# Optimization experiments

Hardware: AMD Instinct MI355X
Metric: run time of the kernel (lower is better)

The kernel has to match this reference:

```python
import jax, jax.numpy as jnp
import numpy as np

S, D_MODEL, D_K = 4096, 1024, 64
SCALE = float(np.sqrt(D_K))


def setup_inputs() -> dict:
    key = jax.random.key(0)
    ks = jax.random.split(key, 7)
    def p(k, shape, fan_in):
        # torch nn.Linear default init: U(-1/sqrt(fan_in), 1/sqrt(fan_in))
        lim = 1.0 / np.sqrt(fan_in)
        return jax.random.uniform(k, shape, jnp.float32, -lim, lim)
    return {
        "x": jax.random.normal(ks[0], (S, D_MODEL), jnp.float32),
        "Wq": p(ks[1], (D_K, D_MODEL), D_MODEL),
        "bq": p(ks[2], (D_K,), D_MODEL),
        "Wk": p(ks[3], (D_K, D_MODEL), D_MODEL),
        "bk": p(ks[4], (D_K,), D_MODEL),
        "Wv": p(ks[5], (D_K, D_MODEL), D_MODEL),
        "bv": p(ks[6], (D_K,), D_MODEL),
    }


def reference(x, Wq, bq, Wk, bk, Wv, bv):
    # Linear projections: y = x @ W.T + b  (torch nn.Linear convention)
    Q = x @ Wq.T + bq          # [S, d_k]
    K = x @ Wk.T + bk          # [S, d_k]
    V = x @ Wv.T + bv          # [S, d_k]
    scores = (Q @ K.T) / SCALE  # [S, S]
    # causal mask: -inf strictly above the diagonal (triu(1))
    row = jnp.arange(S)[:, None]
    col = jnp.arange(S)[None, :]
    scores = jnp.where(col > row, -jnp.inf, scores)
    attn = jax.nn.softmax(scores, axis=1)
    return attn @ V            # [S, d_k]
```

## Files before the change

kernel.cpp:

```cpp
#include <hip/hip_runtime.h>

#define SS 4096
#define DM 1024

typedef __attribute__((ext_vector_type(4))) float f32x4;
typedef __attribute__((ext_vector_type(8))) __bf16 bf16x8;
typedef __attribute__((ext_vector_type(8))) unsigned short ushort8;
typedef __attribute__((ext_vector_type(4))) unsigned short ushort4v;

#define NEGHUGE -3.0e38f
#define LOG2E 1.44269504f

__device__ __forceinline__ unsigned short f2b(float f) {
    unsigned u = __builtin_bit_cast(unsigned, f);
    u += 0x7fffu + ((u >> 16) & 1u);
    return (unsigned short)(u >> 16);
}

__device__ __forceinline__ f32x4 mfma16(ushort8 a, ushort8 b, f32x4 c) {
    return __builtin_amdgcn_mfma_f32_16x16x32_bf16(
        __builtin_bit_cast(bf16x8, a), __builtin_bit_cast(bf16x8, b), c, 0, 0, 0);
}

__global__ __launch_bounds__(256) void convw_kernel(
    const float* __restrict__ Wq, const float* __restrict__ Wk,
    const float* __restrict__ Wv, unsigned short* __restrict__ wb)
{
    int i = (blockIdx.x * 256 + threadIdx.x) * 4;
    const float* src;
    if (i < 65536) src = Wq + i;
    else if (i < 131072) src = Wk + (i - 65536);
    else src = Wv + (i - 131072);
    f32x4 v = *reinterpret_cast<const f32x4*>(src);
    ushort4v o;
    o[0] = f2b(v[0]); o[1] = f2b(v[1]); o[2] = f2b(v[2]); o[3] = f2b(v[3]);
    *reinterpret_cast<ushort4v*>(wb + i) = o;
}

__global__ __launch_bounds__(512) void proj_kernel(
    const float* __restrict__ x, const unsigned short* __restrict__ wb,
    const float* __restrict__ bq, const float* __restrict__ bk, const float* __restrict__ bv,
    unsigned short* __restrict__ Qs, unsigned short* __restrict__ Kb,
    unsigned short* __restrict__ VT)
{
    __shared__ float comb[8 * 3072];
    const int m0 = blockIdx.x * 16;
    const int tid = threadIdx.x;
    const int w = tid >> 6, l = tid & 63;
    const int lc = l & 15;
    const int lk = (l >> 4) * 8;

    f32x4 acc[12] = {};
    const float* xrow = x + (m0 + lc) * DM;
    const int kbase = w * 128;

    for (int kk = 0; kk < 128; kk += 32) {
        const int k0 = kbase + kk + lk;
        f32x4 u = *reinterpret_cast<const f32x4*>(xrow + k0);
        f32x4 v = *reinterpret_cast<const f32x4*>(xrow + k0 + 4);
        ushort8 a;
        a[0] = f2b(u[0]); a[1] = f2b(u[1]); a[2] = f2b(u[2]); a[3] = f2b(u[3]);
        a[4] = f2b(v[0]); a[5] = f2b(v[1]); a[6] = f2b(v[2]); a[7] = f2b(v[3]);
#pragma unroll
        for (int nf = 0; nf < 12; nf++) {
            ushort8 b = *reinterpret_cast<const ushort8*>(wb + (nf * 16 + lc) * DM + k0);
            acc[nf] = mfma16(a, b, acc[nf]);
        }
    }

#pragma unroll
    for (int nf = 0; nf < 12; nf++)
#pragma unroll
        for (int r = 0; r < 4; r++) {
            int row = (l >> 4) * 4 + r;
            comb[w * 3072 + row * 192 + nf * 16 + lc] = acc[nf][r];
        }
    __syncthreads();

    for (int idx = tid; idx < 3072; idx += 512) {
        int row = idx / 192, col = idx % 192;
        float s = 0.f;
#pragma unroll
        for (int ww = 0; ww < 8; ww++) s += comb[ww * 3072 + idx];
        int grow = m0 + row;
        if (col < 64) {
            s += bq[col];
            Qs[grow * 64 + col] = f2b(s * 0.125f);
        } else if (col < 128) {
            s += bk[col - 64];
            Kb[grow * 64 + col - 64] = f2b(s);
        } else {
            s += bv[col - 128];
            VT[(col - 128) * SS + grow] = f2b(s);
        }
    }
}

__global__ __launch_bounds__(256) void attn_part_kernel(
    const unsigned short* __restrict__ Qs, const unsigned short* __restrict__ Kb,
    const unsigned short* __restrict__ VT, float* __restrict__ part)
{
    __shared__ unsigned short plds[4][16 * 64];
    __shared__ float comb[4][16 * 66];

    const int bid = blockIdx.x;
    const int g = bid >> 2, c = bid & 3;
    const int q0 = g * 16;
    const int tid = threadIdx.x;
    const int w = tid >> 6, l = tid & 63;
    const int lc = l & 15;
    const int lg4 = l >> 4;
    const int lk = lg4 * 8;

    const int T = g / 4 + 1;
    const int W0 = c * 4 + w;

    ushort8 aq0 = *reinterpret_cast<const ushort8*>(Qs + (q0 + lc) * 64 + lk);
    ushort8 aq1 = *reinterpret_cast<const ushort8*>(Qs + (q0 + lc) * 64 + 32 + lk);

    float m4[4], l4[4];
    f32x4 o[4] = {};
#pragma unroll
    for (int r = 0; r < 4; r++) { m4[r] = NEGHUGE; l4[r] = 0.f; }

    char* myp = reinterpret_cast<char*>(plds[w]);

    for (int t = W0; t < T; t += 16) {
        const int kv0 = t * 64;
        f32x4 s[4] = {};
#pragma unroll
        for (int nf = 0; nf < 4; nf++) {
            const unsigned short* kr = Kb + (kv0 + nf * 16 + lc) * 64;
            ushort8 b0 = *reinterpret_cast<const ushort8*>(kr + lk);
            ushort8 b1 = *reinterpret_cast<const ushort8*>(kr + 32 + lk);
            s[nf] = mfma16(aq0, b0, s[nf]);
            s[nf] = mfma16(aq1, b1, s[nf]);
        }
        if (kv0 + 63 > q0) {
#pragma unroll
            for (int nf = 0; nf < 4; nf++)
#pragma unroll
                for (int r = 0; r < 4; r++) {
                    int colg = kv0 + nf * 16 + lc;
                    int rowg = q0 + lg4 * 4 + r;
                    if (colg > rowg) s[nf][r] = NEGHUGE;
                }
        }
#pragma unroll
        for (int r = 0; r < 4; r++) {
            float mx = fmaxf(fmaxf(s[0][r], s[1][r]), fmaxf(s[2][r], s[3][r]));
            mx = fmaxf(mx, __shfl_xor(mx, 1));
            mx = fmaxf(mx, __shfl_xor(mx, 2));
            mx = fmaxf(mx, __shfl_xor(mx, 4));
            mx = fmaxf(mx, __shfl_xor(mx, 8));
            float mn = fmaxf(m4[r], mx);
            float sc = exp2f((m4[r] - mn) * LOG2E);
            m4[r] = mn;
            float rs = 0.f;
#pragma unroll
            for (int nf = 0; nf < 4; nf++) {
                float p = exp2f((s[nf][r] - mn) * LOG2E);
                s[nf][r] = p;
                rs += p;
            }
            rs += __shfl_xor(rs, 1);
            rs += __shfl_xor(rs, 2);
            rs += __shfl_xor(rs, 4);
            rs += __shfl_xor(rs, 8);
            l4[r] = l4[r] * sc + rs;
            o[0][r] *= sc; o[1][r] *= sc; o[2][r] *= sc; o[3][r] *= sc;
        }
#pragma unroll
        for (int nf = 0; nf < 4; nf++)
#pragma unroll
            for (int r = 0; r < 4; r++) {
                int row = lg4 * 4 + r;
                int byte = (row * 128 + (nf * 16 + lc) * 2) ^ ((row & 7) << 4);
                *reinterpret_cast<unsigned short*>(myp + byte) = f2b(s[nf][r]);
            }
        asm volatile("s_waitcnt lgkmcnt(0)" ::: "memory");
        __builtin_amdgcn_sched_barrier(0);
#pragma unroll
        for (int k = 0; k < 2; k++) {
            int rbyte = (lc * 128 + (k * 32 + lk) * 2) ^ ((lc & 7) << 4);
            ushort8 pa = *reinterpret_cast<const ushort8*>(myp + rbyte);
#pragma unroll
            for (int df = 0; df < 4; df++) {
                ushort8 bv = *reinterpret_cast<const ushort8*>(
                    VT + (df * 16 + lc) * SS + kv0 + k * 32 + lk);
                o[df] = mfma16(pa, bv, o[df]);
            }
        }
    }

#pragma unroll
    for (int df = 0; df < 4; df++)
#pragma unroll
        for (int r = 0; r < 4; r++)
            comb[w][(lg4 * 4 + r) * 66 + df * 16 + lc] = o[df][r];
    if (lc == 0) {
#pragma unroll
        for (int r = 0; r < 4; r++) {
            comb[w][(lg4 * 4 + r) * 66 + 64] = m4[r];
            comb[w][(lg4 * 4 + r) * 66 + 65] = l4[r];
        }
    }
    __syncthreads();

    float* pp = part + bid * 1056;
    for (int idx = tid; idx < 1024; idx += 256) {
        int row = idx >> 6, col = idx & 63;
        float M = fmaxf(fmaxf(comb[0][row * 66 + 64], comb[1][row * 66 + 64]),
                        fmaxf(comb[2][row * 66 + 64], comb[3][row * 66 + 64]));
        float val = 0.f, den = 0.f;
#pragma unroll
        for (int ww = 0; ww < 4; ww++) {
            float f = exp2f((comb[ww][row * 66 + 64] - M) * LOG2E);
            val += comb[ww][row * 66 + col] * f;
            den += comb[ww][row * 66 + 65] * f;
        }
        pp[row * 66 + col] = val;
        if (col == 0) {
            pp[row * 66 + 64] = M;
            pp[row * 66 + 65] = den;
        }
    }
}

__global__ __launch_bounds__(256) void attn_comb_kernel(
    const float* __restrict__ part, float* __restrict__ out)
{
    const int g = blockIdx.x;
    const int q0 = g * 16;
    const float* p0 = part + (g * 4) * 1056;
    for (int idx = threadIdx.x; idx < 1024; idx += 256) {
        int row = idx >> 6, col = idx & 63;
        float M = NEGHUGE;
#pragma unroll
        for (int cc = 0; cc < 4; cc++)
            M = fmaxf(M, p0[cc * 1056 + row * 66 + 64]);
        float val = 0.f, den = 0.f;
#pragma unroll
        for (int cc = 0; cc < 4; cc++) {
            float f = exp2f((p0[cc * 1056 + row * 66 + 64] - M) * LOG2E);
            val += p0[cc * 1056 + row * 66 + col] * f;
            den += p0[cc * 1056 + row * 66 + 65] * f;
        }
        out[(q0 + row) * 64 + col] = val / den;
    }
}

extern "C" void kernel_launch(void* const* d_in, const int* in_sizes, int n_in,
                              void* d_out, int out_size, void* d_ws, size_t ws_size,
                              hipStream_t stream) {
    const float* x  = (const float*)d_in[0];
    const float* Wq = (const float*)d_in[1];
    const float* bq = (const float*)d_in[2];
    const float* Wk = (const float*)d_in[3];
    const float* bk = (const float*)d_in[4];
    const float* Wv = (const float*)d_in[5];
    const float* bv = (const float*)d_in[6];
    float* out = (float*)d_out;

    char* ws = (char*)d_ws;
    unsigned short* wb = (unsigned short*)ws;
    unsigned short* Qs = (unsigned short*)(ws + 393216);
    unsigned short* Kb = (unsigned short*)(ws + 917504);
    unsigned short* VT = (unsigned short*)(ws + 1441792);
    float* part = (float*)(ws + 1966080);

    convw_kernel<<<dim3(192), dim3(256), 0, stream>>>(Wq, Wk, Wv, wb);
    proj_kernel<<<dim3(256), dim3(512), 0, stream>>>(x, wb, bq, bk, bv, Qs, Kb, VT);
    attn_part_kernel<<<dim3(1024), dim3(256), 0, stream>>>(Qs, Kb, VT, part);
    attn_comb_kernel<<<dim3(256), dim3(256), 0, stream>>>(part, out);
}
```

Baseline: 56.03 us.

## Split projection over feature groups, transpose attention MFMA layout, reverse block order

The projection kernel now runs 1024 smaller blocks of 256 threads, each computing 48 output features over a 16-row tile, instead of 256 blocks computing all 192. This cuts the shared-memory reduction size and raises occupancy, at the cost of reading x four times. The attention kernel computes S transposed so that each lane holds one query row, which removes most of the cross-lane shuffles. It prefetches V fragments before the softmax, packs P with padded LDS stores, and launches the heaviest causal query groups first to improve load balance.

```diff
diff --git a/kernel.cpp b/kernel.cpp
--- a/kernel.cpp
+++ b/kernel.cpp
@@ -2,11 +2,13 @@
 
 #define SS 4096
 #define DM 1024
+#define PSTRIDE 1056
 
 typedef __attribute__((ext_vector_type(4))) float f32x4;
 typedef __attribute__((ext_vector_type(8))) __bf16 bf16x8;
 typedef __attribute__((ext_vector_type(8))) unsigned short ushort8;
 typedef __attribute__((ext_vector_type(4))) unsigned short ushort4v;
+typedef __attribute__((ext_vector_type(2))) unsigned int uint2v;
 
 #define NEGHUGE -3.0e38f
 #define LOG2E 1.44269504f
@@ -37,24 +39,28 @@
     *reinterpret_cast<ushort4v*>(wb + i) = o;
 }
 
-__global__ __launch_bounds__(512) void proj_kernel(
+__global__ __launch_bounds__(256) void proj_kernel(
     const float* __restrict__ x, const unsigned short* __restrict__ wb,
     const float* __restrict__ bq, const float* __restrict__ bk, const float* __restrict__ bv,
     unsigned short* __restrict__ Qs, unsigned short* __restrict__ Kb,
     unsigned short* __restrict__ VT)
 {
-    __shared__ float comb[8 * 3072];
-    const int m0 = blockIdx.x * 16;
+    __shared__ float comb[4 * 16 * 52];
+    const int bid = blockIdx.x;
+    const int m0 = (bid >> 2) * 16;
+    const int fg = bid & 3;
     const int tid = threadIdx.x;
     const int w = tid >> 6, l = tid & 63;
     const int lc = l & 15;
-    const int lk = (l >> 4) * 8;
-
-    f32x4 acc[12] = {};
+    const int lg4 = l >> 4;
+    const int lk = lg4 * 8;
+
+    f32x4 acc[3] = {};
     const float* xrow = x + (m0 + lc) * DM;
-    const int kbase = w * 128;
-
-    for (int kk = 0; kk < 128; kk += 32) {
+    const unsigned short* wbase = wb + (fg * 48 + lc) * DM;
+    const int kbase = w * 256;
+
+    for (int kk = 0; kk < 256; kk += 32) {
         const int k0 = kbase + kk + lk;
         f32x4 u = *reinterpret_cast<const f32x4*>(xrow + k0);
         f32x4 v = *reinterpret_cast<const f32x4*>(xrow + k0 + 4);
@@ -62,36 +68,34 @@
         a[0] = f2b(u[0]); a[1] = f2b(u[1]); a[2] = f2b(u[2]); a[3] = f2b(u[3]);
         a[4] = f2b(v[0]); a[5] = f2b(v[1]); a[6] = f2b(v[2]); a[7] = f2b(v[3]);
 #pragma unroll
-        for (int nf = 0; nf < 12; nf++) {
-            ushort8 b = *reinterpret_cast<const ushort8*>(wb + (nf * 16 + lc) * DM + k0);
+        for (int nf = 0; nf < 3; nf++) {
+            ushort8 b = *reinterpret_cast<const ushort8*>(wbase + nf * 16 * DM + k0);
             acc[nf] = mfma16(a, b, acc[nf]);
         }
     }
 
 #pragma unroll
-    for (int nf = 0; nf < 12; nf++)
-#pragma unroll
-        for (int r = 0; r < 4; r++) {
-            int row = (l >> 4) * 4 + r;
-            comb[w * 3072 + row * 192 + nf * 16 + lc] = acc[nf][r];
-        }
+    for (int nf = 0; nf < 3; nf++)
+#pragma unroll
+        for (int r = 0; r < 4; r++)
+            comb[w * 832 + (lg4 * 4 + r) * 52 + nf * 16 + lc] = acc[nf][r];
     __syncthreads();
 
-    for (int idx = tid; idx < 3072; idx += 512) {
-        int row = idx / 192, col = idx % 192;
-        float s = 0.f;
-#pragma unroll
-        for (int ww = 0; ww < 8; ww++) s += comb[ww * 3072 + idx];
+    for (int idx = tid; idx < 768; idx += 256) {
+        int row = idx / 48, col = idx % 48;
+        int off = row * 52 + col;
+        float s = comb[off] + comb[832 + off] + comb[1664 + off] + comb[2496 + off];
         int grow = m0 + row;
-        if (col < 64) {
-            s += bq[col];
-            Qs[grow * 64 + col] = f2b(s * 0.125f);
-        } else if (col < 128) {
-            s += bk[col - 64];
-            Kb[grow * 64 + col - 64] = f2b(s);
+        int gcol = fg * 48 + col;
+        if (gcol < 64) {
+            s += bq[gcol];
+            Qs[grow * 64 + gcol] = f2b(s * 0.125f);
+        } else if (gcol < 128) {
+            s += bk[gcol - 64];
+            Kb[grow * 64 + gcol - 64] = f2b(s);
         } else {
-            s += bv[col - 128];
-            VT[(col - 128) * SS + grow] = f2b(s);
+            s += bv[gcol - 128];
+            VT[(gcol - 128) * SS + grow] = f2b(s);
         }
     }
 }
@@ -100,11 +104,12 @@
     const unsigned short* __restrict__ Qs, const unsigned short* __restrict__ Kb,
     const unsigned short* __restrict__ VT, float* __restrict__ part)
 {
-    __shared__ unsigned short plds[4][16 * 64];
-    __shared__ float comb[4][16 * 66];
+    __shared__ __align__(16) char plds[4 * 2304];
+    __shared__ float scomb[4][16 * 66];
 
     const int bid = blockIdx.x;
-    const int g = bid >> 2, c = bid & 3;
+    const int g = 255 - (bid >> 2);
+    const int c = bid & 3;
     const int q0 = g * 16;
     const int tid = threadIdx.x;
     const int w = tid >> 6, l = tid & 63;
@@ -118,12 +123,10 @@
     ushort8 aq0 = *reinterpret_cast<const ushort8*>(Qs + (q0 + lc) * 64 + lk);
     ushort8 aq1 = *reinterpret_cast<const ushort8*>(Qs + (q0 + lc) * 64 + 32 + lk);
 
-    float m4[4], l4[4];
+    float m4 = NEGHUGE, l4 = 0.f;
     f32x4 o[4] = {};
-#pragma unroll
-    for (int r = 0; r < 4; r++) { m4[r] = NEGHUGE; l4[r] = 0.f; }
-
-    char* myp = reinterpret_cast<char*>(plds[w]);
+
+    char* myp = plds + w * 2304;
 
     for (int t = W0; t < T; t += 16) {
         const int kv0 = t * 64;
@@ -133,63 +136,68 @@
             const unsigned short* kr = Kb + (kv0 + nf * 16 + lc) * 64;
             ushort8 b0 = *reinterpret_cast<const ushort8*>(kr + lk);
             ushort8 b1 = *reinterpret_cast<const ushort8*>(kr + 32 + lk);
-            s[nf] = mfma16(aq0, b0, s[nf]);
-            s[nf] = mfma16(aq1, b1, s[nf]);
-        }
+            s[nf] = mfma16(b0, aq0, s[nf]);
+            s[nf] = mfma16(b1, aq1, s[nf]);
+        }
+        ushort8 av[2][4];
+#pragma unroll
+        for (int cc = 0; cc < 2; cc++)
+#pragma unroll
+            for (int df = 0; df < 4; df++)
+                av[cc][df] = *reinterpret_cast<const ushort8*>(
+                    VT + (df * 16 + lc) * SS + kv0 + cc * 32 + lk);
+
         if (kv0 + 63 > q0) {
 #pragma unroll
             for (int nf = 0; nf < 4; nf++)
 #pragma unroll
                 for (int r = 0; r < 4; r++) {
-                    int colg = kv0 + nf * 16 + lc;
-                    int rowg = q0 + lg4 * 4 + r;
-                    if (colg > rowg) s[nf][r] = NEGHUGE;
+                    int kvi = kv0 + nf * 16 + lg4 * 4 + r;
+                    if (kvi > q0 + lc) s[nf][r] = NEGHUGE;
                 }
         }
-#pragma unroll
-        for (int r = 0; r < 4; r++) {
-            float mx = fmaxf(fmaxf(s[0][r], s[1][r]), fmaxf(s[2][r], s[3][r]));
-            mx = fmaxf(mx, __shfl_xor(mx, 1));
-            mx = fmaxf(mx, __shfl_xor(mx, 2));
-            mx = fmaxf(mx, __shfl_xor(mx, 4));
-            mx = fmaxf(mx, __shfl_xor(mx, 8));
-            float mn = fmaxf(m4[r], mx);
-            float sc = exp2f((m4[r] - mn) * LOG2E);
-            m4[r] = mn;
-            float rs = 0.f;
-#pragma unroll
-            for (int nf = 0; nf < 4; nf++) {
+        float mx01 = fmaxf(fmaxf(s[0][0], s[0][1]), fmaxf(s[0][2], s[0][3]));
+        float mx11 = fmaxf(fmaxf(s[1][0], s[1][1]), fmaxf(s[1][2], s[1][3]));
+        float mx21 = fmaxf(fmaxf(s[2][0], s[2][1]), fmaxf(s[2][2], s[2][3]));
+        float mx31 = fmaxf(fmaxf(s[3][0], s[3][1]), fmaxf(s[3][2], s[3][3]));
+        float mx = fmaxf(fmaxf(mx01, mx11), fmaxf(mx21, mx31));
+        mx = fmaxf(mx, __shfl_xor(mx, 16));
+        mx = fmaxf(mx, __shfl_xor(mx, 32));
+        float mn = fmaxf(m4, mx);
+        float sc = exp2f((m4 - mn) * LOG2E);
+        m4 = mn;
+        float rs = 0.f;
+#pragma unroll
+        for (int nf = 0; nf < 4; nf++)
+#pragma unroll
+            for (int r = 0; r < 4; r++) {
                 float p = exp2f((s[nf][r] - mn) * LOG2E);
                 s[nf][r] = p;
                 rs += p;
             }
-            rs += __shfl_xor(rs, 1);
-            rs += __shfl_xor(rs, 2);
-            rs += __shfl_xor(rs, 4);
-            rs += __shfl_xor(rs, 8);
-            l4[r] = l4[r] * sc + rs;
-            o[0][r] *= sc; o[1][r] *= sc; o[2][r] *= sc; o[3][r] *= sc;
-        }
-#pragma unroll
-        for (int nf = 0; nf < 4; nf++)
-#pragma unroll
-            for (int r = 0; r < 4; r++) {
-                int row = lg4 * 4 + r;
-                int byte = (row * 128 + (nf * 16 + lc) * 2) ^ ((row & 7) << 4);
-                *reinterpret_cast<unsigned short*>(myp + byte) = f2b(s[nf][r]);
-            }
+        rs += __shfl_xor(rs, 16);
+        rs += __shfl_xor(rs, 32);
+        l4 = l4 * sc + rs;
+#pragma unroll
+        for (int df = 0; df < 4; df++) {
+            o[df][0] *= sc; o[df][1] *= sc; o[df][2] *= sc; o[df][3] *= sc;
+        }
+#pragma unroll
+        for (int nf = 0; nf < 4; nf++) {
+            unsigned p01 = (unsigned)f2b(s[nf][0]) | ((unsigned)f2b(s[nf][1]) << 16);
+            unsigned p23 = (unsigned)f2b(s[nf][2]) | ((unsigned)f2b(s[nf][3]) << 16);
+            uint2v pk; pk[0] = p01; pk[1] = p23;
+            *reinterpret_cast<uint2v*>(myp + lc * 144 + (nf * 8 + lg4 * 2) * 4) = pk;
+        }
         asm volatile("s_waitcnt lgkmcnt(0)" ::: "memory");
         __builtin_amdgcn_sched_barrier(0);
 #pragma unroll
-        for (int k = 0; k < 2; k++) {
-            int rbyte = (lc * 128 + (k * 32 + lk) * 2) ^ ((lc & 7) << 4);
-            ushort8 pa = *reinterpret_cast<const ushort8*>(myp + rbyte);
-#pragma unroll
-            for (int df = 0; df < 4; df++) {
-                ushort8 bv = *reinterpret_cast<const ushort8*>(
-                    VT + (df * 16 + lc) * SS + kv0 + k * 32 + lk);
-                o[df] = mfma16(pa, bv, o[df]);
-            }
+        for (int cc = 0; cc < 2; cc++) {
+            int S = 16 * cc + 4 * lg4;
+            ushort8 pb = *reinterpret_cast<const ushort8*>(myp + lc * 144 + S * 4);
+#pragma unroll
+            for (int df = 0; df < 4; df++)
+                o[df] = mfma16(av[cc][df], pb, o[df]);
         }
     }
 
@@ -197,27 +205,24 @@
     for (int df = 0; df < 4; df++)
 #pragma unroll
         for (int r = 0; r < 4; r++)
-            comb[w][(lg4 * 4 + r) * 66 + df * 16 + lc] = o[df][r];
-    if (lc == 0) {
-#pragma unroll
-        for (int r = 0; r < 4; r++) {
-            comb[w][(lg4 * 4 + r) * 66 + 64] = m4[r];
-            comb[w][(lg4 * 4 + r) * 66 + 65] = l4[r];
-        }
+            scomb[w][lc * 66 + df * 16 + lg4 * 4 + r] = o[df][r];
+    if (lg4 == 0) {
+        scomb[w][lc * 66 + 64] = m4;
+        scomb[w][lc * 66 + 65] = l4;
     }
     __syncthreads();
 
-    float* pp = part + bid * 1056;
+    float* pp = part + bid * PSTRIDE;
     for (int idx = tid; idx < 1024; idx += 256) {
         int row = idx >> 6, col = idx & 63;
-        float M = fmaxf(fmaxf(comb[0][row * 66 + 64], comb[1][row * 66 + 64]),
-                        fmaxf(comb[2][row * 66 + 64], comb[3][row * 66 + 64]));
+        float M = fmaxf(fmaxf(scomb[0][row * 66 + 64], scomb[1][row * 66 + 64]),
+                        fmaxf(scomb[2][row * 66 + 64], scomb[3][row * 66 + 64]));
         float val = 0.f, den = 0.f;
 #pragma unroll
         for (int ww = 0; ww < 4; ww++) {
-            float f = exp2f((comb[ww][row * 66 + 64] - M) * LOG2E);
-            val += comb[ww][row * 66 + col] * f;
-            den += comb[ww][row * 66 + 65] * f;
+            float f = exp2f((scomb[ww][row * 66 + 64] - M) * LOG2E);
+            val += scomb[ww][row * 66 + col] * f;
+            den += scomb[ww][row * 66 + 65] * f;
         }
         pp[row * 66 + col] = val;
         if (col == 0) {
@@ -230,21 +235,22 @@
 __global__ __launch_bounds__(256) void attn_comb_kernel(
     const float* __restrict__ part, float* __restrict__ out)
 {
-    const int g = blockIdx.x;
+    const int b = blockIdx.x;
+    const int g = 255 - b;
     const int q0 = g * 16;
-    const float* p0 = part + (g * 4) * 1056;
+    const float* p0 = part + (b * 4) * PSTRIDE;
     for (int idx = threadIdx.x; idx < 1024; idx += 256) {
         int row = idx >> 6, col = idx & 63;
         float M = NEGHUGE;
 #pragma unroll
         for (int cc = 0; cc < 4; cc++)
-            M = fmaxf(M, p0[cc * 1056 + row * 66 + 64]);
+            M = fmaxf(M, p0[cc * PSTRIDE + row * 66 + 64]);
         float val = 0.f, den = 0.f;
 #pragma unroll
         for (int cc = 0; cc < 4; cc++) {
-            float f = exp2f((p0[cc * 1056 + row * 66 + 64] - M) * LOG2E);
-            val += p0[cc * 1056 + row * 66 + col] * f;
-            den += p0[cc * 1056 + row * 66 + 65] * f;
+            float f = exp2f((p0[cc * PSTRIDE + row * 66 + 64] - M) * LOG2E);
+            val += p0[cc * PSTRIDE + row * 66 + col] * f;
+            den += p0[cc * PSTRIDE + row * 66 + 65] * f;
         }
         out[(q0 + row) * 64 + col] = val / den;
     }
@@ -270,7 +276,7 @@
     float* part = (float*)(ws + 1966080);
 
     convw_kernel<<<dim3(192), dim3(256), 0, stream>>>(Wq, Wk, Wv, wb);
-    proj_kernel<<<dim3(256), dim3(512), 0, stream>>>(x, wb, bq, bk, bv, Qs, Kb, VT);
+    proj_kernel<<<dim3(1024), dim3(256), 0, stream>>>(x, wb, bq, bk, bv, Qs, Kb, VT);
     attn_part_kernel<<<dim3(1024), dim3(256), 0, stream>>>(Qs, Kb, VT, part);
     attn_comb_kernel<<<dim3(256), dim3(256), 0, stream>>>(part, out);
 }
```

Result: slower. 59.61 us (+6.4%).
